# Kernel tuning notes

Hardware: AMD Instinct MI355X
Metric: run time of the kernel (lower is better)

Reference implementation:

```python
import jax, jax.numpy as jnp
import numpy as np

SITE, DIM = 8, 16
B = 8192
D = 2 * DIM

# --- static Z2-graded (Grassmann) bookkeeping -------------------------------
# Each edge (d, d) has parity 0 for the first d indices, parity 1 for the rest.
# Merging two graded edges reorders the flat product index so that all
# even-parity combinations come first (stable/lex within each sector).

def _merge_order(pA, pB):
    p = (pA[:, None] ^ pB[None, :]).reshape(-1)
    return np.argsort(p, kind='stable')

_P1 = np.array([0, 1])                                        # edge (1,1)
_PD = np.concatenate([np.zeros(DIM, np.int64), np.ones(DIM, np.int64)])  # edge (d,d)
ORDER_DD = _merge_order(_PD, _PD); INV_DD = np.argsort(ORDER_DD)
ORDER_1D = _merge_order(_P1, _PD); INV_1D = np.argsort(ORDER_1D)
ORDER_11 = _merge_order(_P1, _P1)                             # = [0,3,1,2]
MASK_X = jnp.asarray((_P1[:, None] ^ _PD[None, :]) == 0, jnp.float32)   # (2, D)
MASK_G2 = jnp.asarray((_PD[:, None] ^ _PD[None, :]) == 0, jnp.float32)  # (D, D)
MASK_G3 = jnp.asarray((_PD[:, None, None] ^ _PD[None, :, None] ^ _PD[None, None, :]) == 0, jnp.float32)
SIGN_PD = jnp.asarray(1.0 - 2.0 * _PD, jnp.float32)           # (-1)^parity, reverse sign
SWSIGN = jnp.asarray((-1.0) ** (_P1[:, None] * _PD[None, :]), jnp.float32)  # swap sign (2, D)


def setup_inputs() -> dict:
    key = jax.random.key(0)
    k1, k2, k3, k4 = jax.random.split(key, 4)
    return {
        'data': jax.random.randint(k1, (B, SITE), 0, 2),
        'embedding': jax.random.normal(k2, (SITE, 2, DIM), jnp.float32),
        'head_w': jax.random.normal(k3, (D, D), jnp.float32),
        'body_w': jax.random.normal(k4, (SITE - 1, D, D, D), jnp.float32),
    }


def _embed(emb_table, bits):
    # emb_table: (2, DIM); bits: (B,) in {0,1}
    emb = emb_table[bits]                                     # (B, DIM)
    zero = jnp.zeros_like(emb)
    on = bits[:, None] != 0
    row0 = jnp.concatenate([jnp.where(on, 0.0, emb), zero], -1)   # slot 0 (even,even)
    row1 = jnp.concatenate([zero, jnp.where(on, emb, 0.0)], -1)   # slot 3 (odd,odd)
    return jnp.stack([row0, row1], 1) * MASK_X                # (B, 2, D), even parity


def _body(x1, x2, g3):
    # x1, x2: (B, 2, D); g3: (D, D, D) with arrows (T, T, F)
    b = x1.shape[0]
    g = g3 * MASK_G3
    g = g * SIGN_PD[None, :, None]                            # reverse axis 1 (arrow flip)
    g_m = g.reshape(D, D * D)[:, ORDER_DD]                    # merge axes 1,2 even-first
    gx1 = jnp.einsum('bsk,km->bsm', x1 * MASK_X, g_m)         # (B, 2, D*D)
    gx1 = gx1[..., INV_DD].reshape(b, 2, D, D)                # split merged edge back
    gx1 = gx1 * SIGN_PD[None, None, :, None]                  # reverse axis 2
    gx1 = gx1 * SWSIGN[None, :, :, None]                      # graded sign: swap axes 1,2
    gx1_m = jnp.transpose(gx1, (0, 2, 1, 3)).reshape(b, D, 2 * D)[..., ORDER_1D]
    gx12 = jnp.einsum('bsk,bkm->bsm', x2 * MASK_X, gx1_m)     # (B, 2, 2D)
    gx12 = gx12[..., INV_1D].reshape(b, 2, 2, D)              # split into (s1 edge, (d,d))
    gx12 = gx12.reshape(b, 4, D)[:, ORDER_11, :]              # merge (s2, s1) even-first
    return gx12.reshape(b, 2, 2, D).sum(2)                    # sum per parity sector -> (B, 2, D)


def reference(data, embedding, head_w, body_w):
    x = _embed(embedding[0], data[:, 0])
    x = jnp.tanh(jnp.einsum('bsk,kj->bsj', x, head_w * MASK_G2))
    for i in range(1, SITE):
        x = jnp.tanh(_body(x, _embed(embedding[i], data[:, i]), body_w[i - 1]))
    return x
```

## Files before the change

kernel.cpp:

```cpp
#include <hip/hip_runtime.h>
#include <cmath>

#define SITE 8
#define DIM 16
#define BATCH 8192

#define WS_M   0
#define WS_HV  7168
#define WS_PAT 8192

__device__ __forceinline__ float fast_tanh(float a) {
    float t = __expf(2.0f * a);
    return 1.0f - 2.0f / (t + 1.0f);
}

__global__ __launch_bounds__(256) void build_kernel(
    const float* __restrict__ embedding,
    const float* __restrict__ head_w,
    const float* __restrict__ body_w,
    float* __restrict__ ws)
{
    const int tid = threadIdx.x;
    if (blockIdx.x < 7) {
        int t = blockIdx.x * 256 + tid;
        int r = t >> 6;
        int rem = t & 63;
        int k  = rem >> 2;
        int j4 = rem & 3;
        int s   = r >> 2;
        int bit = (r >> 1) & 1;
        int h   = r & 1;
        int rowoff = (bit ^ h) << 4;
        int ioff   = bit << 4;
        int coloff = (h << 4) + j4 * 4;
        float sgn  = (bit && !h) ? -1.0f : 1.0f;
        const float* g3  = body_w + s * 32768 + (k + rowoff) * 1024 + ioff * 32 + coloff;
        const float* emb = embedding + (s + 1) * 32 + bit * 16;
        float4 acc = make_float4(0.f, 0.f, 0.f, 0.f);
        #pragma unroll
        for (int i = 0; i < 16; ++i) {
            float e = emb[i];
            float4 g = *(const float4*)(g3 + i * 32);
            acc.x += e * g.x; acc.y += e * g.y; acc.z += e * g.z; acc.w += e * g.w;
        }
        acc.x *= sgn; acc.y *= sgn; acc.z *= sgn; acc.w *= sgn;
        *(float4*)(ws + WS_M + r * 256 + k * 16 + j4 * 4) = acc;
    } else {
        if (tid < 32) {
            int h = tid >> 4;
            int j = tid & 15;
            const float* emb = embedding + h * 16;
            float a = 0.f;
            if (h == 0) {
                #pragma unroll
                for (int k = 0; k < 16; ++k) a += emb[k] * head_w[k * 32 + j];
            } else {
                #pragma unroll
                for (int k = 0; k < 16; ++k) a += emb[k] * head_w[(k + 16) * 32 + (j + 16)];
            }
            ws[WS_HV + h * 16 + j] = fast_tanh(a);
        }
    }
}

__global__ __launch_bounds__(256) void recur_kernel(
    const float* __restrict__ ws_in,
    float* __restrict__ ws_out)
{
    __shared__ float Ml[7168];
    __shared__ __align__(16) float st[8][2][16];

    const int tid = threadIdx.x;
    #pragma unroll
    for (int it = 0; it < 7; ++it) {
        int i4 = tid + 256 * it;
        ((float4*)Ml)[i4] = ((const float4*)(ws_in + WS_M))[i4];
    }
    __syncthreads();

    const int pl = tid >> 5;
    const int p  = blockIdx.x * 8 + pl;
    const int h  = (tid >> 4) & 1;
    const int j  = tid & 15;

    float v = ((p & 1) == h) ? ws_in[WS_HV + h * 16 + j] : 0.f;
    st[pl][h][j] = v;

    #pragma unroll
    for (int s = 1; s < SITE; ++s) {
        int bit = (p >> s) & 1;
        const float* src = st[pl][h ^ bit];
        const float* m   = Ml + ((s - 1) * 4 + bit * 2 + h) * 256;
        float a = 0.f;
        #pragma unroll
        for (int k = 0; k < 16; ++k) a += src[k] * m[k * 16 + j];
        v = fast_tanh(a);
        st[pl][h][j] = v;
    }

    ws_out[WS_PAT + p * 32 + h * 16 + j] = v;
}

__global__ __launch_bounds__(256) void scatter_kernel(
    const int* __restrict__ data,
    const float4* __restrict__ pat4,
    float4* __restrict__ out4)
{
    int gid = blockIdx.x * 256 + threadIdx.x;
    int b = gid >> 4;
    int q = gid & 15;
    const int4* d4 = (const int4*)(data + b * 8);
    int4 w0 = d4[0];
    int4 w1 = d4[1];
    int id = (w0.x & 1) | ((w0.y & 1) << 1) | ((w0.z & 1) << 2) | ((w0.w & 1) << 3)
           | ((w1.x & 1) << 4) | ((w1.y & 1) << 5) | ((w1.z & 1) << 6) | ((w1.w & 1) << 7);
    float4 v = make_float4(0.f, 0.f, 0.f, 0.f);
    if (q < 4)        v = pat4[id * 8 + q];
    else if (q >= 12) v = pat4[id * 8 + (q - 8)];
    out4[b * 16 + q] = v;
}

extern "C" void kernel_launch(void* const* d_in, const int* in_sizes, int n_in,
                              void* d_out, int out_size, void* d_ws, size_t ws_size,
                              hipStream_t stream) {
    const int*   data      = (const int*)d_in[0];
    const float* embedding = (const float*)d_in[1];
    const float* head_w    = (const float*)d_in[2];
    const float* body_w    = (const float*)d_in[3];
    float* ws = (float*)d_ws;

    build_kernel<<<8, 256, 0, stream>>>(embedding, head_w, body_w, ws);
    recur_kernel<<<32, 256, 0, stream>>>(ws, ws);
    scatter_kernel<<<(BATCH * 16) / 256, 256, 0, stream>>>(
        data, (const float4*)(ws + WS_PAT), (float4*)d_out);
}
```

Measured before the change: 67.22 us.

## Fuse recurrence and scatter into one per-batch kernel with padded LDS matrices

Merges the pattern-recurrence kernel and the scatter kernel into a single kernel that runs the 7-step recurrence directly for each batch row's bit pattern. Results go straight to the output, with no intermediate pattern table in workspace. This drops a kernel launch and the round trip through global memory. The build step now stores the site matrices with padded strides to avoid LDS bank conflicts, and the dot product uses four accumulators. The cost is that 8192 rows are each recomputed instead of 256 unique patterns, and all 1024 blocks reload the roughly 30KB matrix set into LDS.

After: 66.37 us. No clear change (-1.3%).

```diff
diff --git a/kernel.cpp b/kernel.cpp
--- a/kernel.cpp
+++ b/kernel.cpp
@@ -5,9 +5,10 @@
 #define DIM 16
 #define BATCH 8192
 
-#define WS_M   0
-#define WS_HV  7168
-#define WS_PAT 8192
+#define WS_MPAD 272
+#define WS_KPAD 17
+#define WS_MEND 7616
+#define WS_HV   7616
 
 __device__ __forceinline__ float fast_tanh(float a) {
     float t = __expf(2.0f * a);
@@ -43,8 +44,9 @@
             float4 g = *(const float4*)(g3 + i * 32);
             acc.x += e * g.x; acc.y += e * g.y; acc.z += e * g.z; acc.w += e * g.w;
         }
-        acc.x *= sgn; acc.y *= sgn; acc.z *= sgn; acc.w *= sgn;
-        *(float4*)(ws + WS_M + r * 256 + k * 16 + j4 * 4) = acc;
+        float* dst = ws + r * WS_MPAD + k * WS_KPAD + j4 * 4;
+        dst[0] = sgn * acc.x; dst[1] = sgn * acc.y;
+        dst[2] = sgn * acc.z; dst[3] = sgn * acc.w;
     } else {
         if (tid < 32) {
             int h = tid >> 4;
@@ -63,61 +65,65 @@
     }
 }
 
-__global__ __launch_bounds__(256) void recur_kernel(
-    const float* __restrict__ ws_in,
-    float* __restrict__ ws_out)
+__global__ __launch_bounds__(256) void recur_scatter_kernel(
+    const int* __restrict__ data,
+    const float* __restrict__ ws,
+    float4* __restrict__ out4)
 {
-    __shared__ float Ml[7168];
+    __shared__ __align__(16) float Ml[WS_MEND];
     __shared__ __align__(16) float st[8][2][16];
 
     const int tid = threadIdx.x;
+
     #pragma unroll
-    for (int it = 0; it < 7; ++it) {
+    for (int it = 0; it < 8; ++it) {
         int i4 = tid + 256 * it;
-        ((float4*)Ml)[i4] = ((const float4*)(ws_in + WS_M))[i4];
+        if (i4 < WS_MEND / 4)
+            ((float4*)Ml)[i4] = ((const float4*)ws)[i4];
     }
-    __syncthreads();
 
     const int pl = tid >> 5;
-    const int p  = blockIdx.x * 8 + pl;
     const int h  = (tid >> 4) & 1;
     const int j  = tid & 15;
+    const int b  = blockIdx.x * 8 + pl;
 
-    float v = ((p & 1) == h) ? ws_in[WS_HV + h * 16 + j] : 0.f;
-    st[pl][h][j] = v;
+    float hvv = ws[WS_HV + h * 16 + j];
 
-    #pragma unroll
-    for (int s = 1; s < SITE; ++s) {
-        int bit = (p >> s) & 1;
-        const float* src = st[pl][h ^ bit];
-        const float* m   = Ml + ((s - 1) * 4 + bit * 2 + h) * 256;
-        float a = 0.f;
-        #pragma unroll
-        for (int k = 0; k < 16; ++k) a += src[k] * m[k * 16 + j];
-        v = fast_tanh(a);
-        st[pl][h][j] = v;
-    }
-
-    ws_out[WS_PAT + p * 32 + h * 16 + j] = v;
-}
-
-__global__ __launch_bounds__(256) void scatter_kernel(
-    const int* __restrict__ data,
-    const float4* __restrict__ pat4,
-    float4* __restrict__ out4)
-{
-    int gid = blockIdx.x * 256 + threadIdx.x;
-    int b = gid >> 4;
-    int q = gid & 15;
     const int4* d4 = (const int4*)(data + b * 8);
     int4 w0 = d4[0];
     int4 w1 = d4[1];
     int id = (w0.x & 1) | ((w0.y & 1) << 1) | ((w0.z & 1) << 2) | ((w0.w & 1) << 3)
            | ((w1.x & 1) << 4) | ((w1.y & 1) << 5) | ((w1.z & 1) << 6) | ((w1.w & 1) << 7);
-    float4 v = make_float4(0.f, 0.f, 0.f, 0.f);
-    if (q < 4)        v = pat4[id * 8 + q];
-    else if (q >= 12) v = pat4[id * 8 + (q - 8)];
-    out4[b * 16 + q] = v;
+
+    __syncthreads();
+
+    float v = ((id & 1) == h) ? hvv : 0.f;
+    st[pl][h][j] = v;
+
+    #pragma unroll
+    for (int s = 1; s < SITE; ++s) {
+        int bit = (id >> s) & 1;
+        const float* src = st[pl][h ^ bit];
+        const float* m   = Ml + ((s - 1) * 4 + bit * 2 + h) * WS_MPAD;
+        float a0 = 0.f, a1 = 0.f, a2 = 0.f, a3 = 0.f;
+        #pragma unroll
+        for (int k = 0; k < 16; k += 4) {
+            a0 += src[k]     * m[k * WS_KPAD + j];
+            a1 += src[k + 1] * m[(k + 1) * WS_KPAD + j];
+            a2 += src[k + 2] * m[(k + 2) * WS_KPAD + j];
+            a3 += src[k + 3] * m[(k + 3) * WS_KPAD + j];
+        }
+        v = fast_tanh((a0 + a1) + (a2 + a3));
+        st[pl][h][j] = v;
+    }
+
+    if ((tid & 31) < 16) {
+        int q = j;
+        float4 v4 = make_float4(0.f, 0.f, 0.f, 0.f);
+        if (q < 4)        v4 = *(const float4*)&st[pl][0][q * 4];
+        else if (q >= 12) v4 = *(const float4*)&st[pl][1][(q - 12) * 4];
+        out4[b * 16 + q] = v4;
+    }
 }
 
 extern "C" void kernel_launch(void* const* d_in, const int* in_sizes, int n_in,
@@ -130,7 +136,5 @@
     float* ws = (float*)d_ws;
 
     build_kernel<<<8, 256, 0, stream>>>(embedding, head_w, body_w, ws);
-    recur_kernel<<<32, 256, 0, stream>>>(ws, ws);
-    scatter_kernel<<<(BATCH * 16) / 256, 256, 0, stream>>>(
-        data, (const float4*)(ws + WS_PAT), (float4*)d_out);
+    recur_scatter_kernel<<<BATCH / 8, 256, 0, stream>>>(data, ws, (float4*)d_out);
 }
```
